# Kernel optimization log

Hardware: AMD Instinct MI355X
Metric: run time of the kernel (lower is better)

The kernel has to match this reference:

```python
import jax, jax.numpy as jnp
import numpy as np

LN_EPS = 1e-5

def _layernorm(x, g, b):
    mu = jnp.mean(x, axis=-1, keepdims=True)
    var = jnp.mean((x - mu) ** 2, axis=-1, keepdims=True)
    return (x - mu) * jax.lax.rsqrt(var + LN_EPS) * g + b

def _mlp(x, w0, b0, wh, bh, lng, lnb, wout, bout):
    # Linear -> ReLU -> LN, repeated; final Linear.
    h = _layernorm(jax.nn.relu(x @ w0.T + b0), lng[0], lnb[0])
    for i in range(wh.shape[0]):
        h = _layernorm(jax.nn.relu(h @ wh[i].T + bh[i]), lng[i + 1], lnb[i + 1])
    return h @ wout.T + bout

def _vq(z, codebook, commitment_cost=0.25):
    B, A, D = z.shape
    flat = z.reshape(-1, D)                                  # [N, D]
    d = (jnp.sum(flat ** 2, axis=1, keepdims=True)
         + jnp.sum(codebook ** 2, axis=1)
         - 2.0 * flat @ codebook.T)                          # [N, K]
    idx = jnp.argmin(d, axis=1)                              # [N]
    quantized = codebook[idx].reshape(z.shape)               # gather, not one-hot matmul
    e_latent = jnp.mean((jax.lax.stop_gradient(quantized) - z) ** 2)
    q_latent = jnp.mean((quantized - jax.lax.stop_gradient(z)) ** 2)
    vq_loss = commitment_cost * e_latent + q_latent
    quantized = z + jax.lax.stop_gradient(quantized - z)     # straight-through
    return quantized, vq_loss

def setup_inputs() -> dict:
    key = jax.random.key(0)
    ks = jax.random.split(key, 8)
    H, D, K = 256, 64, 512
    B, A = 2048, 128
    s = lambda fan_in: 1.0 / np.sqrt(fan_in)
    return {
        'x': jax.random.normal(ks[0], (B, A, 3), jnp.float32),
        'enc_w0': jax.random.normal(ks[1], (H, 3), jnp.float32) * s(3),
        'enc_b0': jnp.zeros((H,), jnp.float32),
        'enc_wh': jax.random.normal(ks[2], (2, H, H), jnp.float32) * s(H),
        'enc_bh': jnp.zeros((2, H), jnp.float32),
        'enc_ln_g': jnp.ones((3, H), jnp.float32),
        'enc_ln_b': jnp.zeros((3, H), jnp.float32),
        'enc_wout': jax.random.normal(ks[3], (D, H), jnp.float32) * s(H),
        'enc_bout': jnp.zeros((D,), jnp.float32),
        'codebook': jax.random.uniform(ks[4], (K, D), jnp.float32, -1.0 / K, 1.0 / K),
        'dec_w0': jax.random.normal(ks[5], (H, D), jnp.float32) * s(D),
        'dec_b0': jnp.zeros((H,), jnp.float32),
        'dec_wh': jax.random.normal(ks[6], (2, H, H), jnp.float32) * s(H),
        'dec_bh': jnp.zeros((2, H), jnp.float32),
        'dec_ln_g': jnp.ones((3, H), jnp.float32),
        'dec_ln_b': jnp.zeros((3, H), jnp.float32),
        'dec_wout': jax.random.normal(ks[7], (3, H), jnp.float32) * s(H),
        'dec_bout': jnp.zeros((3,), jnp.float32),
    }

def reference(x, enc_w0, enc_b0, enc_wh, enc_bh, enc_ln_g, enc_ln_b, enc_wout, enc_bout,
              codebook, dec_w0, dec_b0, dec_wh, dec_bh, dec_ln_g, dec_ln_b, dec_wout, dec_bout):
    z = _mlp(x, enc_w0, enc_b0, enc_wh, enc_bh, enc_ln_g, enc_ln_b, enc_wout, enc_bout)
    quantized, vq_loss = _vq(z, codebook)
    recon = _mlp(quantized, dec_w0, dec_b0, dec_wh, dec_bh, dec_ln_g, dec_ln_b, dec_wout, dec_bout)
    loss = jnp.mean((recon - x) ** 2) + vq_loss
    return recon, quantized, loss
```

## Files before the change

kernel.cpp:

```cpp
#include <hip/hip_runtime.h>
#include <math.h>

__device__ __forceinline__ float fma4(float4 w, float4 a, float acc) {
  return fmaf(w.w, a.w, fmaf(w.z, a.z, fmaf(w.y, a.y, fmaf(w.x, a.x, acc))));
}


__device__ __forceinline__ void quadf(const float (*A)[256], int kq, const float4* wbuf,
                                      float* acc, int gr8) {
  float4 a_[8];
  #pragma unroll
  for (int i = 0; i < 8; ++i) a_[i] = *(const float4*)&A[gr8 + i][kq * 4];
  #pragma unroll
  for (int kk = 0; kk < 4; ++kk) {
    const float4 wlo = wbuf[kk * 2], whi = wbuf[kk * 2 + 1];
    #pragma unroll
    for (int i = 0; i < 8; ++i) {
      const float av = kk == 0 ? a_[i].x : kk == 1 ? a_[i].y : kk == 2 ? a_[i].z : a_[i].w;
      acc[i * 8 + 0] = fmaf(av, wlo.x, acc[i * 8 + 0]);
      acc[i * 8 + 1] = fmaf(av, wlo.y, acc[i * 8 + 1]);
      acc[i * 8 + 2] = fmaf(av, wlo.z, acc[i * 8 + 2]);
      acc[i * 8 + 3] = fmaf(av, wlo.w, acc[i * 8 + 3]);
      acc[i * 8 + 4] = fmaf(av, whi.x, acc[i * 8 + 4]);
      acc[i * 8 + 5] = fmaf(av, whi.y, acc[i * 8 + 5]);
      acc[i * 8 + 6] = fmaf(av, whi.z, acc[i * 8 + 6]);
      acc[i * 8 + 7] = fmaf(av, whi.w, acc[i * 8 + 7]);
    }
  }
}

template <int NKQ>
__device__ __forceinline__ void gemm256(const float (*A)[256], const float* __restrict__ WT,
                                        float* acc, int gr8, int c0) {
  #pragma unroll
  for (int i = 0; i < 64; ++i) acc[i] = 0.f;
  float4 wA[8], wB[8];
  #pragma unroll
  for (int kk = 0; kk < 4; ++kk) {
    wA[kk * 2]     = *(const float4*)&WT[(size_t)kk * 256 + c0];
    wA[kk * 2 + 1] = *(const float4*)&WT[(size_t)kk * 256 + c0 + 4];
  }
  #pragma unroll 1
  for (int kq = 0; kq < NKQ; kq += 2) {
    #pragma unroll
    for (int kk = 0; kk < 4; ++kk) {
      wB[kk * 2]     = *(const float4*)&WT[(size_t)((kq + 1) * 4 + kk) * 256 + c0];
      wB[kk * 2 + 1] = *(const float4*)&WT[(size_t)((kq + 1) * 4 + kk) * 256 + c0 + 4];
    }
    quadf(A, kq, wA, acc, gr8);
    if (kq + 2 < NKQ) {
      #pragma unroll
      for (int kk = 0; kk < 4; ++kk) {
        wA[kk * 2]     = *(const float4*)&WT[(size_t)((kq + 2) * 4 + kk) * 256 + c0];
        wA[kk * 2 + 1] = *(const float4*)&WT[(size_t)((kq + 2) * 4 + kk) * 256 + c0 + 4];
      }
    }
    quadf(A, kq + 1, wB, acc, gr8);
  }
}

__device__ __forceinline__ void bias_relu(float* acc, const float* __restrict__ Bp, int c0) {
  float bv[8];
  *(float4*)&bv[0] = *(const float4*)&Bp[c0];
  *(float4*)&bv[4] = *(const float4*)&Bp[c0 + 4];
  #pragma unroll
  for (int rr = 0; rr < 8; ++rr)
    #pragma unroll
    for (int c = 0; c < 8; ++c)
      acc[rr * 8 + c] = fmaxf(acc[rr * 8 + c] + bv[c], 0.f);
}

__device__ __forceinline__ void ln64g(float* acc, float* P36,
                                      const float* __restrict__ gg,
                                      const float* __restrict__ bb,
                                      int l, int gr8, int c0) {
  const int ls = l & 31;
  float mu[8];
  #pragma unroll
  for (int rr = 0; rr < 8; ++rr) {
    const float* a = &acc[rr * 8];
    P36[(gr8 + rr) * 36 + ls] =
        (((a[0] + a[1]) + (a[2] + a[3])) + ((a[4] + a[5]) + (a[6] + a[7])));
  }
  __syncthreads();
  if (l < 16) {
    float q[8];
    #pragma unroll
    for (int j = 0; j < 8; ++j) {
      const float4 u = *(const float4*)&P36[l * 36 + 4 * j];
      q[j] = (u.x + u.y) + (u.z + u.w);
    }
    const float s = ((q[0] + q[1]) + (q[2] + q[3])) + ((q[4] + q[5]) + (q[6] + q[7]));
    P36[l * 36 + 32] = s * (1.f / 256.f);
  }
  __syncthreads();
  #pragma unroll
  for (int rr = 0; rr < 8; ++rr) mu[rr] = P36[(gr8 + rr) * 36 + 32];
  __syncthreads();
  #pragma unroll
  for (int rr = 0; rr < 8; ++rr) {
    const float* a = &acc[rr * 8];
    const float m = mu[rr];
    const float d0 = a[0] - m, d1 = a[1] - m, d2 = a[2] - m, d3 = a[3] - m;
    const float d4 = a[4] - m, d5 = a[5] - m, d6 = a[6] - m, d7 = a[7] - m;
    float s = d0 * d0;
    s = fmaf(d1, d1, s); s = fmaf(d2, d2, s); s = fmaf(d3, d3, s);
    s = fmaf(d4, d4, s); s = fmaf(d5, d5, s); s = fmaf(d6, d6, s); s = fmaf(d7, d7, s);
    P36[(gr8 + rr) * 36 + ls] = s;
  }
  __syncthreads();
  if (l < 16) {
    float q[8];
    #pragma unroll
    for (int j = 0; j < 8; ++j) {
      const float4 u = *(const float4*)&P36[l * 36 + 4 * j];
      q[j] = (u.x + u.y) + (u.z + u.w);
    }
    const float s2 = ((q[0] + q[1]) + (q[2] + q[3])) + ((q[4] + q[5]) + (q[6] + q[7]));
    P36[l * 36 + 32] = 1.f / sqrtf(s2 * (1.f / 256.f) + 1e-5f);
  }
  __syncthreads();
  float gv[8], bv[8];
  *(float4*)&gv[0] = *(const float4*)&gg[c0];
  *(float4*)&gv[4] = *(const float4*)&gg[c0 + 4];
  *(float4*)&bv[0] = *(const float4*)&bb[c0];
  *(float4*)&bv[4] = *(const float4*)&bb[c0 + 4];
  #pragma unroll
  for (int rr = 0; rr < 8; ++rr) {
    const float rs = P36[(gr8 + rr) * 36 + 32];
    const float m = mu[rr];
    #pragma unroll
    for (int c = 0; c < 8; ++c)
      acc[rr * 8 + c] = ((acc[rr * 8 + c] - m) * rs) * gv[c] + bv[c];
  }
}

__device__ __forceinline__ void storeA64g(float (*A)[256], const float* acc, int gr8, int c0) {
  #pragma unroll
  for (int rr = 0; rr < 8; ++rr) {
    *(float4*)&A[gr8 + rr][c0] =
        make_float4(acc[rr * 8], acc[rr * 8 + 1], acc[rr * 8 + 2], acc[rr * 8 + 3]);
    *(float4*)&A[gr8 + rr][c0 + 4] =
        make_float4(acc[rr * 8 + 4], acc[rr * 8 + 5], acc[rr * 8 + 6], acc[rr * 8 + 7]);
  }
}

__global__ __launch_bounds__(64, 2) void k_mlp(
    const float* __restrict__ x, const float* __restrict__ w0, const float* __restrict__ b0,
    const float* __restrict__ wt1, const float* __restrict__ wt2, const float* __restrict__ bh,
    const float* __restrict__ lng, const float* __restrict__ lnb,
    const float* __restrict__ wtout, const float* __restrict__ bout, float* __restrict__ z,
    const float* __restrict__ cb, const float* __restrict__ wt0d, const float* __restrict__ db0,
    const float* __restrict__ wtd1, const float* __restrict__ wtd2, const float* __restrict__ dbh,
    const float* __restrict__ dlng, const float* __restrict__ dlnb,
    const float* __restrict__ dwout, const float* __restrict__ dbout,
    float* __restrict__ table, float* __restrict__ ne) {
  __shared__ float A[16][256];
  float* Pa = &A[0][0];
  const int l = threadIdx.x;
  const int gr8 = (l >> 5) * 8;
  const int c0 = (l & 31) * 8;
  float acc[64];

  if (blockIdx.x >= 32) {
    const size_t rbase = (size_t)(blockIdx.x - 32) * 16;
    {
      float wv[24], bv[8];
      #pragma unroll
      for (int i = 0; i < 6; ++i) *(float4*)&wv[i * 4] = *(const float4*)&w0[c0 * 3 + i * 4];
      *(float4*)&bv[0] = *(const float4*)&b0[c0];
      *(float4*)&bv[4] = *(const float4*)&b0[c0 + 4];
      #pragma unroll
      for (int rr = 0; rr < 8; ++rr) {
        const size_t r3 = (rbase + gr8 + rr) * 3;
        const float x0 = x[r3], x1 = x[r3 + 1], x2 = x[r3 + 2];
        #pragma unroll
        for (int c = 0; c < 8; ++c) {
          const float s = fmaf(wv[c * 3 + 2], x2, fmaf(wv[c * 3 + 1], x1, wv[c * 3] * x0));
          acc[rr * 8 + c] = fmaxf(s + bv[c], 0.f);
        }
      }
    }
    ln64g(acc, Pa, lng, lnb, l, gr8, c0);
    storeA64g(A, acc, gr8, c0);
    __syncthreads();

    gemm256<64>(A, wt1, acc, gr8, c0);
    bias_relu(acc, bh, c0);
    ln64g(acc, Pa, lng + 256, lnb + 256, l, gr8, c0);
    __syncthreads();
    storeA64g(A, acc, gr8, c0);
    __syncthreads();

    gemm256<64>(A, wt2, acc, gr8, c0);
    bias_relu(acc, bh + 256, c0);
    ln64g(acc, Pa, lng + 512, lnb + 512, l, gr8, c0);
    __syncthreads();
    storeA64g(A, acc, gr8, c0);
    __syncthreads();

    {
      const int c0o = (l & 31) * 2;
      float o[16];
      #pragma unroll
      for (int i = 0; i < 16; ++i) o[i] = 0.f;
      #pragma unroll 1
      for (int kq = 0; kq < 64; ++kq) {
        float4 a[8];
        #pragma unroll
        for (int i = 0; i < 8; ++i) a[i] = *(const float4*)&A[gr8 + i][kq * 4];
        #pragma unroll
        for (int kk = 0; kk < 4; ++kk) {
          const float2 wv = *(const float2*)&wtout[(size_t)(kq * 4 + kk) * 64 + c0o];
          #pragma unroll
          for (int i = 0; i < 8; ++i) {
            const float av = kk == 0 ? a[i].x : kk == 1 ? a[i].y : kk == 2 ? a[i].z : a[i].w;
            o[i * 2]     = fmaf(av, wv.x, o[i * 2]);
            o[i * 2 + 1] = fmaf(av, wv.y, o[i * 2 + 1]);
          }
        }
      }
      const float2 bb = *(const float2*)&bout[c0o];
      #pragma unroll
      for (int rr = 0; rr < 8; ++rr) {
        float2 st;
        st.x = o[rr * 2] + bb.x;
        st.y = o[rr * 2 + 1] + bb.y;
        *(float2*)&z[(rbase + gr8 + rr) * 64 + c0o] = st;
      }
    }
  } else {
    const int cbase = blockIdx.x * 16;
    if (l < 16) {
      float s = 0.f;
      #pragma unroll 8
      for (int k = 0; k < 64; ++k) {
        const float v = cb[(size_t)(cbase + l) * 64 + k];
        s = fmaf(v, v, s);
      }
      ne[cbase + l] = s;
    }
    {
      const float4* cbf = (const float4*)(cb + (size_t)cbase * 64);
      const int r = l >> 2, q = l & 3;
      #pragma unroll
      for (int i = 0; i < 4; ++i)
        *(float4*)&A[r][q * 16 + i * 4] = cbf[r * 16 + q * 4 + i];
    }
    __syncthreads();

    gemm256<16>(A, wt0d, acc, gr8, c0);
    bias_relu(acc, db0, c0);
    ln64g(acc, Pa, dlng, dlnb, l, gr8, c0);
    __syncthreads();
    storeA64g(A, acc, gr8, c0);
    __syncthreads();

    gemm256<64>(A, wtd1, acc, gr8, c0);
    bias_relu(acc, dbh, c0);
    ln64g(acc, Pa, dlng + 256, dlnb + 256, l, gr8, c0);
    __syncthreads();
    storeA64g(A, acc, gr8, c0);
    __syncthreads();

    gemm256<64>(A, wtd2, acc, gr8, c0);
    bias_relu(acc, dbh + 256, c0);
    ln64g(acc, Pa, dlng + 512, dlnb + 512, l, gr8, c0);
    __syncthreads();
    storeA64g(A, acc, gr8, c0);
    __syncthreads();

    if (l < 16) {
      #pragma unroll
      for (int j = 0; j < 3; ++j) {
        float s = 0.f;
        #pragma unroll 4
        for (int kq = 0; kq < 64; ++kq) {
          const float4 w = *(const float4*)&dwout[j * 256 + kq * 4];
          const float4 a = *(const float4*)&A[l][kq * 4];
          s = fma4(w, a, s);
        }
        table[(cbase + l) * 3 + j] = s + dbout[j];
      }
    }
  }
}

__global__ __launch_bounds__(256) void k_wt(
    const float* __restrict__ wh, const float* __restrict__ wout,
    const float* __restrict__ dwh, const float* __restrict__ dw0,
    float* __restrict__ wt1, float* __restrict__ wt2, float* __restrict__ wtout,
    float* __restrict__ wtd1, float* __restrict__ wtd2, float* __restrict__ wt0d) {
  const int b = blockIdx.x, t = threadIdx.x;
  if (b < 256) {
    wt1[b * 256 + t] = wh[t * 256 + b];
  } else if (b < 512) {
    const int k = b - 256;
    wt2[k * 256 + t] = wh[65536 + t * 256 + k];
  } else if (b < 576) {
    const int k = (b - 512) * 4 + (t >> 6);
    const int j = t & 63;
    wtout[k * 64 + j] = wout[j * 256 + k];
  } else if (b < 832) {
    const int k = b - 576;
    wtd1[k * 256 + t] = dwh[t * 256 + k];
  } else if (b < 1088) {
    const int k = b - 832;
    wtd2[k * 256 + t] = dwh[65536 + t * 256 + k];
  } else {
    const int k = b - 1088;
    wt0d[k * 256 + t] = dw0[t * 64 + k];
  }
}

__global__ __launch_bounds__(256) void k_vq(
    float* __restrict__ zq_io, const float* __restrict__ cb,
    const float* __restrict__ ne, const float* __restrict__ table,
    const float* __restrict__ x, float* __restrict__ recon,
    float* __restrict__ psr, float* __restrict__ psv) {
  __shared__ float red[256];
  const int t = threadIdx.x;
  const int row = blockIdx.x * 256 + t;
  float4 zf[16];
  {
    const float4* zp = (const float4*)(zq_io + (size_t)row * 64);
    #pragma unroll
    for (int q = 0; q < 16; ++q) zf[q] = zp[q];
  }
  float nz = 0.f;
  #pragma unroll
  for (int q = 0; q < 16; ++q) {
    nz = fmaf(zf[q].x, zf[q].x, nz);
    nz = fmaf(zf[q].y, zf[q].y, nz);
    nz = fmaf(zf[q].z, zf[q].z, nz);
    nz = fmaf(zf[q].w, zf[q].w, nz);
  }
  float dmin = INFINITY; int imin = 0;
  const float4* cbv = (const float4*)cb;
  for (int c = 0; c < 512; ++c) {
    float da = 0.f, db = 0.f;
    #pragma unroll
    for (int q = 0; q < 16; q += 2) {
      const float4 ea = cbv[c * 16 + q];
      const float4 eb = cbv[c * 16 + q + 1];
      da = fmaf(ea.x, zf[q].x, da);
      da = fmaf(ea.y, zf[q].y, da);
      da = fmaf(ea.z, zf[q].z, da);
      da = fmaf(ea.w, zf[q].w, da);
      db = fmaf(eb.x, zf[q + 1].x, db);
      db = fmaf(eb.y, zf[q + 1].y, db);
      db = fmaf(eb.z, zf[q + 1].z, db);
      db = fmaf(eb.w, zf[q + 1].w, db);
    }
    const float dot = da + db;
    const float d = (nz + ne[c]) - 2.f * dot;
    if (d < dmin) { dmin = d; imin = c; }
  }
  float sv = 0.f;
  {
    const float4* eq = (const float4*)(cb + imin * 64);
    float4* qo = (float4*)(zq_io + (size_t)row * 64);
    #pragma unroll
    for (int q = 0; q < 16; ++q) {
      const float4 e = eq[q];
      const float4 zz = zf[q];
      const float ax = e.x - zz.x, ay = e.y - zz.y, az = e.z - zz.z, aw = e.w - zz.w;
      sv = fmaf(ax, ax, sv); sv = fmaf(ay, ay, sv);
      sv = fmaf(az, az, sv); sv = fmaf(aw, aw, sv);
      float4 st;
      st.x = zz.x + ax; st.y = zz.y + ay; st.z = zz.z + az; st.w = zz.w + aw;
      qo[q] = st;
    }
  }
  const float r0 = table[imin * 3], r1 = table[imin * 3 + 1], r2 = table[imin * 3 + 2];
  recon[row * 3] = r0; recon[row * 3 + 1] = r1; recon[row * 3 + 2] = r2;
  const float e0 = r0 - x[row * 3], e1 = r1 - x[row * 3 + 1], e2 = r2 - x[row * 3 + 2];
  const float sr = fmaf(e2, e2, fmaf(e1, e1, e0 * e0));
  red[t] = sr; __syncthreads();
  #pragma unroll
  for (int o = 128; o > 0; o >>= 1) { if (t < o) red[t] += red[t + o]; __syncthreads(); }
  if (t == 0) psr[blockIdx.x] = red[0];
  __syncthreads();
  red[t] = sv; __syncthreads();
  #pragma unroll
  for (int o = 128; o > 0; o >>= 1) { if (t < o) red[t] += red[t + o]; __syncthreads(); }
  if (t == 0) psv[blockIdx.x] = red[0];
}

__global__ __launch_bounds__(256) void k_loss(
    const float* __restrict__ psr, const float* __restrict__ psv,
    float* __restrict__ out) {
  __shared__ float ra[256], rb[256];
  const int t = threadIdx.x;
  const float sr = ((psr[t] + psr[t + 256]) + psr[t + 512]) + psr[t + 768];
  const float sv = ((psv[t] + psv[t + 256]) + psv[t + 512]) + psv[t + 768];
  ra[t] = sr; rb[t] = sv;
  __syncthreads();
  #pragma unroll
  for (int o = 128; o > 0; o >>= 1) {
    if (t < o) { ra[t] += ra[t + o]; rb[t] += rb[t + o]; }
    __syncthreads();
  }
  if (t == 0) {
    const float mr = ra[0] / 786432.f;
    const float mv = rb[0] * (1.f / 16777216.f);
    const float vq = 0.25f * mv + mv;
    out[0] = mr + vq;
  }
}

extern "C" void kernel_launch(void* const* d_in, const int* in_sizes, int n_in,
                              void* d_out, int out_size, void* d_ws, size_t ws_size,
                              hipStream_t stream) {
  const float* x        = (const float*)d_in[0];
  const float* enc_w0   = (const float*)d_in[1];
  const float* enc_b0   = (const float*)d_in[2];
  const float* enc_wh   = (const float*)d_in[3];
  const float* enc_bh   = (const float*)d_in[4];
  const float* enc_lng  = (const float*)d_in[5];
  const float* enc_lnb  = (const float*)d_in[6];
  const float* enc_wout = (const float*)d_in[7];
  const float* enc_bout = (const float*)d_in[8];
  const float* cb       = (const float*)d_in[9];
  const float* dec_w0   = (const float*)d_in[10];
  const float* dec_b0   = (const float*)d_in[11];
  const float* dec_wh   = (const float*)d_in[12];
  const float* dec_bh   = (const float*)d_in[13];
  const float* dec_lng  = (const float*)d_in[14];
  const float* dec_lnb  = (const float*)d_in[15];
  const float* dec_wout = (const float*)d_in[16];
  const float* dec_bout = (const float*)d_in[17];

  float* out   = (float*)d_out;
  float* recon = out;
  float* qbuf  = out + 786432;
  float* lossp = out + 786432 + 16777216;

  float* wt1   = out;
  float* wt2   = out + 65536;
  float* wtout = out + 131072;
  float* wtd1  = out + 147456;
  float* wtd2  = out + 212992;
  float* wt0d  = out + 278528;

  float* ws    = (float*)d_ws;
  float* ne    = ws;
  float* table = ws + 512;
  float* psr   = ws + 2048;
  float* psv   = ws + 3072;

  k_wt<<<1152, 256, 0, stream>>>(enc_wh, enc_wout, dec_wh, dec_w0,
                                 wt1, wt2, wtout, wtd1, wtd2, wt0d);
  k_mlp<<<16416, 64, 0, stream>>>(x, enc_w0, enc_b0, wt1, wt2, enc_bh,
                                  enc_lng, enc_lnb, wtout, enc_bout, qbuf,
                                  cb, wt0d, dec_b0, wtd1, wtd2, dec_bh,
                                  dec_lng, dec_lnb, dec_wout, dec_bout,
                                  table, ne);
  k_vq<<<1024, 256, 0, stream>>>(qbuf, cb, ne, table, x, recon, psr, psv);
  k_loss<<<1, 256, 0, stream>>>(psr, psv, lossp);
}
```

Baseline: 1.305 ms.

## Split MLP block work across two wavefronts with smaller per-thread tiles

```diff
diff --git a/kernel.cpp b/kernel.cpp
--- a/kernel.cpp
+++ b/kernel.cpp
@@ -6,56 +6,38 @@
 }
 
 
-__device__ __forceinline__ void quadf(const float (*A)[256], int kq, const float4* wbuf,
-                                      float* acc, int gr8) {
-  float4 a_[8];
-  #pragma unroll
-  for (int i = 0; i < 8; ++i) a_[i] = *(const float4*)&A[gr8 + i][kq * 4];
-  #pragma unroll
-  for (int kk = 0; kk < 4; ++kk) {
-    const float4 wlo = wbuf[kk * 2], whi = wbuf[kk * 2 + 1];
-    #pragma unroll
-    for (int i = 0; i < 8; ++i) {
-      const float av = kk == 0 ? a_[i].x : kk == 1 ? a_[i].y : kk == 2 ? a_[i].z : a_[i].w;
-      acc[i * 8 + 0] = fmaf(av, wlo.x, acc[i * 8 + 0]);
-      acc[i * 8 + 1] = fmaf(av, wlo.y, acc[i * 8 + 1]);
-      acc[i * 8 + 2] = fmaf(av, wlo.z, acc[i * 8 + 2]);
-      acc[i * 8 + 3] = fmaf(av, wlo.w, acc[i * 8 + 3]);
-      acc[i * 8 + 4] = fmaf(av, whi.x, acc[i * 8 + 4]);
-      acc[i * 8 + 5] = fmaf(av, whi.y, acc[i * 8 + 5]);
-      acc[i * 8 + 6] = fmaf(av, whi.z, acc[i * 8 + 6]);
-      acc[i * 8 + 7] = fmaf(av, whi.w, acc[i * 8 + 7]);
-    }
-  }
-}
-
 template <int NKQ>
-__device__ __forceinline__ void gemm256(const float (*A)[256], const float* __restrict__ WT,
-                                        float* acc, int gr8, int c0) {
-  #pragma unroll
-  for (int i = 0; i < 64; ++i) acc[i] = 0.f;
-  float4 wA[8], wB[8];
-  #pragma unroll
-  for (int kk = 0; kk < 4; ++kk) {
-    wA[kk * 2]     = *(const float4*)&WT[(size_t)kk * 256 + c0];
-    wA[kk * 2 + 1] = *(const float4*)&WT[(size_t)kk * 256 + c0 + 4];
-  }
+__device__ __forceinline__ void gemmW(const float (*A)[256], const float* __restrict__ WT,
+                                      float* acc, int r0, int c0) {
+  #pragma unroll
+  for (int i = 0; i < 32; ++i) acc[i] = 0.f;
   #pragma unroll 1
-  for (int kq = 0; kq < NKQ; kq += 2) {
+  for (int kq = 0; kq < NKQ; ++kq) {
+    float4 wv[8];
     #pragma unroll
     for (int kk = 0; kk < 4; ++kk) {
-      wB[kk * 2]     = *(const float4*)&WT[(size_t)((kq + 1) * 4 + kk) * 256 + c0];
-      wB[kk * 2 + 1] = *(const float4*)&WT[(size_t)((kq + 1) * 4 + kk) * 256 + c0 + 4];
-    }
-    quadf(A, kq, wA, acc, gr8);
-    if (kq + 2 < NKQ) {
-      #pragma unroll
-      for (int kk = 0; kk < 4; ++kk) {
-        wA[kk * 2]     = *(const float4*)&WT[(size_t)((kq + 2) * 4 + kk) * 256 + c0];
-        wA[kk * 2 + 1] = *(const float4*)&WT[(size_t)((kq + 2) * 4 + kk) * 256 + c0 + 4];
-      }
-    }
-    quadf(A, kq + 1, wB, acc, gr8);
+      wv[kk * 2]     = *(const float4*)&WT[(size_t)(kq * 4 + kk) * 256 + c0];
+      wv[kk * 2 + 1] = *(const float4*)&WT[(size_t)(kq * 4 + kk) * 256 + c0 + 4];
+    }
+    float4 a_[4];
+    #pragma unroll
+    for (int i = 0; i < 4; ++i) a_[i] = *(const float4*)&A[r0 + i][kq * 4];
+    #pragma unroll
+    for (int kk = 0; kk < 4; ++kk) {
+      const float4 wlo = wv[kk * 2], whi = wv[kk * 2 + 1];
+      #pragma unroll
+      for (int i = 0; i < 4; ++i) {
+        const float av = kk == 0 ? a_[i].x : kk == 1 ? a_[i].y : kk == 2 ? a_[i].z : a_[i].w;
+        acc[i * 8 + 0] = fmaf(av, wlo.x, acc[i * 8 + 0]);
+        acc[i * 8 + 1] = fmaf(av, wlo.y, acc[i * 8 + 1]);
+        acc[i * 8 + 2] = fmaf(av, wlo.z, acc[i * 8 + 2]);
+        acc[i * 8 + 3] = fmaf(av, wlo.w, acc[i * 8 + 3]);
+        acc[i * 8 + 4] = fmaf(av, whi.x, acc[i * 8 + 4]);
+        acc[i * 8 + 5] = fmaf(av, whi.y, acc[i * 8 + 5]);
+        acc[i * 8 + 6] = fmaf(av, whi.z, acc[i * 8 + 6]);
+        acc[i * 8 + 7] = fmaf(av, whi.w, acc[i * 8 + 7]);
+      }
+    }
   }
 }
 
@@ -64,41 +46,42 @@
   *(float4*)&bv[0] = *(const float4*)&Bp[c0];
   *(float4*)&bv[4] = *(const float4*)&Bp[c0 + 4];
   #pragma unroll
-  for (int rr = 0; rr < 8; ++rr)
+  for (int rr = 0; rr < 4; ++rr)
     #pragma unroll
     for (int c = 0; c < 8; ++c)
       acc[rr * 8 + c] = fmaxf(acc[rr * 8 + c] + bv[c], 0.f);
 }
 
-__device__ __forceinline__ void ln64g(float* acc, float* P36,
-                                      const float* __restrict__ gg,
-                                      const float* __restrict__ bb,
-                                      int l, int gr8, int c0) {
-  const int ls = l & 31;
-  float mu[8];
-  #pragma unroll
-  for (int rr = 0; rr < 8; ++rr) {
+__device__ __forceinline__ void ln16(float* acc, float* P36,
+                                     const float* __restrict__ gg,
+                                     const float* __restrict__ bb,
+                                     int t, int r0, int c0) {
+  const int slot = ((t >> 6) << 4) | (t & 15);
+  float mu[4];
+  __syncthreads();
+  #pragma unroll
+  for (int rr = 0; rr < 4; ++rr) {
     const float* a = &acc[rr * 8];
-    P36[(gr8 + rr) * 36 + ls] =
+    P36[(r0 + rr) * 36 + slot] =
         (((a[0] + a[1]) + (a[2] + a[3])) + ((a[4] + a[5]) + (a[6] + a[7])));
   }
   __syncthreads();
-  if (l < 16) {
+  if (t < 16) {
     float q[8];
     #pragma unroll
     for (int j = 0; j < 8; ++j) {
-      const float4 u = *(const float4*)&P36[l * 36 + 4 * j];
+      const float4 u = *(const float4*)&P36[t * 36 + 4 * j];
       q[j] = (u.x + u.y) + (u.z + u.w);
     }
     const float s = ((q[0] + q[1]) + (q[2] + q[3])) + ((q[4] + q[5]) + (q[6] + q[7]));
-    P36[l * 36 + 32] = s * (1.f / 256.f);
-  }
-  __syncthreads();
-  #pragma unroll
-  for (int rr = 0; rr < 8; ++rr) mu[rr] = P36[(gr8 + rr) * 36 + 32];
-  __syncthreads();
-  #pragma unroll
-  for (int rr = 0; rr < 8; ++rr) {
+    P36[t * 36 + 32] = s * (1.f / 256.f);
+  }
+  __syncthreads();
+  #pragma unroll
+  for (int rr = 0; rr < 4; ++rr) mu[rr] = P36[(r0 + rr) * 36 + 32];
+  __syncthreads();
+  #pragma unroll
+  for (int rr = 0; rr < 4; ++rr) {
     const float* a = &acc[rr * 8];
     const float m = mu[rr];
     const float d0 = a[0] - m, d1 = a[1] - m, d2 = a[2] - m, d3 = a[3] - m;
@@ -106,18 +89,18 @@
     float s = d0 * d0;
     s = fmaf(d1, d1, s); s = fmaf(d2, d2, s); s = fmaf(d3, d3, s);
     s = fmaf(d4, d4, s); s = fmaf(d5, d5, s); s = fmaf(d6, d6, s); s = fmaf(d7, d7, s);
-    P36[(gr8 + rr) * 36 + ls] = s;
-  }
-  __syncthreads();
-  if (l < 16) {
+    P36[(r0 + rr) * 36 + slot] = s;
+  }
+  __syncthreads();
+  if (t < 16) {
     float q[8];
     #pragma unroll
     for (int j = 0; j < 8; ++j) {
-      const float4 u = *(const float4*)&P36[l * 36 + 4 * j];
+      const float4 u = *(const float4*)&P36[t * 36 + 4 * j];
       q[j] = (u.x + u.y) + (u.z + u.w);
     }
     const float s2 = ((q[0] + q[1]) + (q[2] + q[3])) + ((q[4] + q[5]) + (q[6] + q[7]));
-    P36[l * 36 + 32] = 1.f / sqrtf(s2 * (1.f / 256.f) + 1e-5f);
+    P36[t * 36 + 32] = 1.f / sqrtf(s2 * (1.f / 256.f) + 1e-5f);
   }
   __syncthreads();
   float gv[8], bv[8];
@@ -126,8 +109,8 @@
   *(float4*)&bv[0] = *(const float4*)&bb[c0];
   *(float4*)&bv[4] = *(const float4*)&bb[c0 + 4];
   #pragma unroll
-  for (int rr = 0; rr < 8; ++rr) {
-    const float rs = P36[(gr8 + rr) * 36 + 32];
+  for (int rr = 0; rr < 4; ++rr) {
+    const float rs = P36[(r0 + rr) * 36 + 32];
     const float m = mu[rr];
     #pragma unroll
     for (int c = 0; c < 8; ++c)
@@ -135,17 +118,17 @@
   }
 }
 
-__device__ __forceinline__ void storeA64g(float (*A)[256], const float* acc, int gr8, int c0) {
-  #pragma unroll
-  for (int rr = 0; rr < 8; ++rr) {
-    *(float4*)&A[gr8 + rr][c0] =
+__device__ __forceinline__ void storeA16(float (*A)[256], const float* acc, int r0, int c0) {
+  #pragma unroll
+  for (int rr = 0; rr < 4; ++rr) {
+    *(float4*)&A[r0 + rr][c0] =
         make_float4(acc[rr * 8], acc[rr * 8 + 1], acc[rr * 8 + 2], acc[rr * 8 + 3]);
-    *(float4*)&A[gr8 + rr][c0 + 4] =
+    *(float4*)&A[r0 + rr][c0 + 4] =
         make_float4(acc[rr * 8 + 4], acc[rr * 8 + 5], acc[rr * 8 + 6], acc[rr * 8 + 7]);
   }
 }
 
-__global__ __launch_bounds__(64, 2) void k_mlp(
+__global__ __launch_bounds__(128, 4) void k_mlp(
     const float* __restrict__ x, const float* __restrict__ w0, const float* __restrict__ b0,
     const float* __restrict__ wt1, const float* __restrict__ wt2, const float* __restrict__ bh,
     const float* __restrict__ lng, const float* __restrict__ lnb,
@@ -157,10 +140,13 @@
     float* __restrict__ table, float* __restrict__ ne) {
   __shared__ float A[16][256];
   float* Pa = &A[0][0];
-  const int l = threadIdx.x;
-  const int gr8 = (l >> 5) * 8;
-  const int c0 = (l & 31) * 8;
-  float acc[64];
+  const int t = threadIdx.x;
+  const int w = t >> 6;
+  const int li = t & 15;
+  const int g = (t >> 4) & 3;
+  const int c0 = w * 128 + li * 8;
+  const int r0 = g * 4;
+  float acc[32];
 
   if (blockIdx.x >= 32) {
     const size_t rbase = (size_t)(blockIdx.x - 32) * 16;
@@ -171,8 +157,8 @@
       *(float4*)&bv[0] = *(const float4*)&b0[c0];
       *(float4*)&bv[4] = *(const float4*)&b0[c0 + 4];
       #pragma unroll
-      for (int rr = 0; rr < 8; ++rr) {
-        const size_t r3 = (rbase + gr8 + rr) * 3;
+      for (int rr = 0; rr < 4; ++rr) {
+        const size_t r3 = (rbase + r0 + rr) * 3;
         const float x0 = x[r3], x1 = x[r3 + 1], x2 = x[r3 + 2];
         #pragma unroll
         for (int c = 0; c < 8; ++c) {
@@ -181,106 +167,105 @@
         }
       }
     }
-    ln64g(acc, Pa, lng, lnb, l, gr8, c0);
-    storeA64g(A, acc, gr8, c0);
-    __syncthreads();
-
-    gemm256<64>(A, wt1, acc, gr8, c0);
+    ln16(acc, Pa, lng, lnb, t, r0, c0);
+    __syncthreads();
+    storeA16(A, acc, r0, c0);
+    __syncthreads();
+
+    gemmW<64>(A, wt1, acc, r0, c0);
     bias_relu(acc, bh, c0);
-    ln64g(acc, Pa, lng + 256, lnb + 256, l, gr8, c0);
-    __syncthreads();
-    storeA64g(A, acc, gr8, c0);
-    __syncthreads();
-
-    gemm256<64>(A, wt2, acc, gr8, c0);
+    ln16(acc, Pa, lng + 256, lnb + 256, t, r0, c0);
+    __syncthreads();
+    storeA16(A, acc, r0, c0);
+    __syncthreads();
+
+    gemmW<64>(A, wt2, acc, r0, c0);
     bias_relu(acc, bh + 256, c0);
-    ln64g(acc, Pa, lng + 512, lnb + 512, l, gr8, c0);
-    __syncthreads();
-    storeA64g(A, acc, gr8, c0);
+    ln16(acc, Pa, lng + 512, lnb + 512, t, r0, c0);
+    __syncthreads();
+    storeA16(A, acc, r0, c0);
     __syncthreads();
 
     {
-      const int c0o = (l & 31) * 2;
-      float o[16];
-      #pragma unroll
-      for (int i = 0; i < 16; ++i) o[i] = 0.f;
+      const int l6 = t & 63;
+      const int col = w * 32 + (l6 & 31);
+      const int rg8 = (l6 >> 5) * 8;
+      float o[8];
+      #pragma unroll
+      for (int i = 0; i < 8; ++i) o[i] = 0.f;
       #pragma unroll 1
       for (int kq = 0; kq < 64; ++kq) {
-        float4 a[8];
+        float4 a_[8];
         #pragma unroll
-        for (int i = 0; i < 8; ++i) a[i] = *(const float4*)&A[gr8 + i][kq * 4];
+        for (int i = 0; i < 8; ++i) a_[i] = *(const float4*)&A[rg8 + i][kq * 4];
         #pragma unroll
         for (int kk = 0; kk < 4; ++kk) {
-          const float2 wv = *(const float2*)&wtout[(size_t)(kq * 4 + kk) * 64 + c0o];
+          const float wv = wtout[(size_t)(kq * 4 + kk) * 64 + col];
           #pragma unroll
           for (int i = 0; i < 8; ++i) {
-            const float av = kk == 0 ? a[i].x : kk == 1 ? a[i].y : kk == 2 ? a[i].z : a[i].w;
-            o[i * 2]     = fmaf(av, wv.x, o[i * 2]);
-            o[i * 2 + 1] = fmaf(av, wv.y, o[i * 2 + 1]);
+            const float av = kk == 0 ? a_[i].x : kk == 1 ? a_[i].y : kk == 2 ? a_[i].z : a_[i].w;
+            o[i] = fmaf(av, wv, o[i]);
           }
         }
       }
-      const float2 bb = *(const float2*)&bout[c0o];
-      #pragma unroll
-      for (int rr = 0; rr < 8; ++rr) {
-        float2 st;
-        st.x = o[rr * 2] + bb.x;
-        st.y = o[rr * 2 + 1] + bb.y;
-        *(float2*)&z[(rbase + gr8 + rr) * 64 + c0o] = st;
-      }
+      const float bb = bout[col];
+      #pragma unroll
+      for (int rr = 0; rr < 8; ++rr)
+        z[(rbase + rg8 + rr) * 64 + col] = o[rr] + bb;
     }
   } else {
     const int cbase = blockIdx.x * 16;
-    if (l < 16) {
+    if (t < 16) {
       float s = 0.f;
       #pragma unroll 8
       for (int k = 0; k < 64; ++k) {
-        const float v = cb[(size_t)(cbase + l) * 64 + k];
+        const float v = cb[(size_t)(cbase + t) * 64 + k];
         s = fmaf(v, v, s);
       }
-      ne[cbase + l] = s;
+      ne[cbase + t] = s;
     }
     {
       const float4* cbf = (const float4*)(cb + (size_t)cbase * 64);
-      const int r = l >> 2, q = l & 3;
-      #pragma unroll
-      for (int i = 0; i < 4; ++i)
-        *(float4*)&A[r][q * 16 + i * 4] = cbf[r * 16 + q * 4 + i];
-    }
-    __syncthreads();
-
-    gemm256<16>(A, wt0d, acc, gr8, c0);
+      #pragma unroll
+      for (int i = 0; i < 2; ++i) {
+        const int j = t * 2 + i;
+        *(float4*)&A[j >> 4][(j & 15) * 4] = cbf[j];
+      }
+    }
+    __syncthreads();
+
+    gemmW<16>(A, wt0d, acc, r0, c0);
     bias_relu(acc, db0, c0);
-    ln64g(acc, Pa, dlng, dlnb, l, gr8, c0);
-    __syncthreads();
-    storeA64g(A, acc, gr8, c0);
-    __syncthreads();
-
-    gemm256<64>(A, wtd1, acc, gr8, c0);
+    ln16(acc, Pa, dlng, dlnb, t, r0, c0);
+    __syncthreads();
+    storeA16(A, acc, r0, c0);
+    __syncthreads();
+
+    gemmW<64>(A, wtd1, acc, r0, c0);
     bias_relu(acc, dbh, c0);
-    ln64g(acc, Pa, dlng + 256, dlnb + 256, l, gr8, c0);
-    __syncthreads();
-    storeA64g(A, acc, gr8, c0);
-    __syncthreads();
-
-    gemm256<64>(A, wtd2, acc, gr8, c0);
+    ln16(acc, Pa, dlng + 256, dlnb + 256, t, r0, c0);
+    __syncthreads();
+    storeA16(A, acc, r0, c0);
+    __syncthreads();
+
+    gemmW<64>(A, wtd2, acc, r0, c0);
     bias_relu(acc, dbh + 256, c0);
-    ln64g(acc, Pa, dlng + 512, dlnb + 512, l, gr8, c0);
-    __syncthreads();
-    storeA64g(A, acc, gr8, c0);
-    __syncthreads();
-
-    if (l < 16) {
+    ln16(acc, Pa, dlng + 512, dlnb + 512, t, r0, c0);
+    __syncthreads();
+    storeA16(A, acc, r0, c0);
+    __syncthreads();
+
+    if (t < 16) {
       #pragma unroll
       for (int j = 0; j < 3; ++j) {
         float s = 0.f;
         #pragma unroll 4
         for (int kq = 0; kq < 64; ++kq) {
-          const float4 w = *(const float4*)&dwout[j * 256 + kq * 4];
-          const float4 a = *(const float4*)&A[l][kq * 4];
-          s = fma4(w, a, s);
+          const float4 wq = *(const float4*)&dwout[j * 256 + kq * 4];
+          const float4 a = *(const float4*)&A[t][kq * 4];
+          s = fma4(wq, a, s);
         }
-        table[(cbase + l) * 3 + j] = s + dbout[j];
+        table[(cbase + t) * 3 + j] = s + dbout[j];
       }
     }
   }
@@ -451,11 +436,11 @@
 
   k_wt<<<1152, 256, 0, stream>>>(enc_wh, enc_wout, dec_wh, dec_w0,
                                  wt1, wt2, wtout, wtd1, wtd2, wt0d);
-  k_mlp<<<16416, 64, 0, stream>>>(x, enc_w0, enc_b0, wt1, wt2, enc_bh,
-                                  enc_lng, enc_lnb, wtout, enc_bout, qbuf,
-                                  cb, wt0d, dec_b0, wtd1, wtd2, dec_bh,
-                                  dec_lng, dec_lnb, dec_wout, dec_bout,
-                                  table, ne);
+  k_mlp<<<16416, 128, 0, stream>>>(x, enc_w0, enc_b0, wt1, wt2, enc_bh,
+                                   enc_lng, enc_lnb, wtout, enc_bout, qbuf,
+                                   cb, wt0d, dec_b0, wtd1, wtd2, dec_bh,
+                                   dec_lng, dec_lnb, dec_wout, dec_bout,
+                                   table, ne);
   k_vq<<<1024, 256, 0, stream>>>(qbuf, cb, ne, table, x, recon, psr, psv);
   k_loss<<<1, 256, 0, stream>>>(psr, psv, lossp);
 }
```

After: 1.455 ms. 11.5% more time.
